# Performance work log

Measured on AMD Instinct MI355X. Metric: run time of the kernel, lower is better.

The kernel has to match this reference:

```python
import jax, jax.numpy as jnp
import numpy as np

V, N, D, HEADS = 4, 1536, 256, 4


def setup_inputs() -> dict:
    key = jax.random.key(0)
    ks = jax.random.split(key, 8)
    s = 0.05  # weight init scale
    return {
        "H": jax.random.normal(ks[0], (V, N, D), jnp.float32),
        "C": jax.random.normal(ks[1], (V, V, N, N), jnp.float32),
        "WQ": jax.random.normal(ks[2], (V, D, D), jnp.float32) * s,
        "WK": jax.random.normal(ks[3], (V, D, D), jnp.float32) * s,
        "WV": jax.random.normal(ks[4], (V, D, D), jnp.float32) * s,
        "in_proj_w": jax.random.normal(ks[5], (3 * D, D), jnp.float32) * s,
        "in_proj_b": jnp.zeros((3 * D,), jnp.float32),
        "out_proj_w": jax.random.normal(ks[6], (D, D), jnp.float32) * s,
        "out_proj_b": jnp.zeros((D,), jnp.float32),
        "alphas": jnp.full((V,), 0.95, jnp.float32),
        "alpha_align": jnp.asarray(0.5, jnp.float32),
        "beta": jnp.asarray(0.5, jnp.float32),
        "topk": 32,
    }


def _ircva(H, in_proj_w, in_proj_b, out_proj_w, out_proj_b, alphas):
    # torch MultiheadAttention, seq=V, batch=N, embed=D, heads=HEADS
    dh = D // HEADS
    qkv = jnp.einsum('snd,ed->sne', H, in_proj_w) + in_proj_b  # (V,N,3D)
    q, k, v = jnp.split(qkv, 3, axis=-1)
    q = q.reshape(V, N, HEADS, dh)
    k = k.reshape(V, N, HEADS, dh)
    v = v.reshape(V, N, HEADS, dh)
    att = jnp.einsum('snhd,tnhd->nhst', q, k) / jnp.sqrt(jnp.float32(dh))
    w = jax.nn.softmax(att, axis=-1)
    o = jnp.einsum('nhst,tnhd->snhd', w, v).reshape(V, N, D)
    fusion = jnp.einsum('snd,ed->sne', o, out_proj_w) + out_proj_b
    a = alphas[:, None, None]
    return fusion * a + (1.0 - a) * H  # (V,N,D)


def _crcva(aligned, C, WQ, WK, WV, K):
    # per-view projections: Linear y = x @ W.T
    Qn = jnp.einsum('vnd,ved->vne', aligned, WQ)
    Kn = jnp.einsum('vnd,ved->vne', aligned, WK)
    Vn = jnp.einsum('vnd,ved->vne', aligned, WV)
    # per-row top-k sparsification of C[p,q]
    vals, idx = jax.lax.top_k(C, K)  # (V,V,N,K)
    Cf = C.reshape(-1, N)
    rows = jnp.arange(Cf.shape[0])[:, None]
    sparse = jnp.zeros_like(Cf).at[rows, idx.reshape(-1, K)].set(vals.reshape(-1, K))
    sparse = sparse.reshape(V, V, N, N)
    row_sum = sparse.sum(axis=-1, keepdims=True) + 1e-12
    C_hat = sparse / row_sum
    # diagonal (p==q) pairs are left as zeros in the torch code
    offdiag = (1.0 - jnp.eye(V, dtype=C.dtype))[:, :, None, None]
    C_hat = C_hat * offdiag
    mask = (C_hat > 0).astype(C.dtype)
    scores = jnp.einsum('pnd,qmd->pqnm', Qn, Kn) / jnp.sqrt(jnp.float32(D))
    scores = scores * mask + (1.0 - mask) * (-1e9)
    alpha_nbr = jax.nn.softmax(scores, axis=-1)
    return jnp.einsum('pqnm,qmd->pnd', alpha_nbr, Vn)  # (V,N,D)


def reference(H, C, WQ, WK, WV, in_proj_w, in_proj_b, out_proj_w, out_proj_b,
              alphas, alpha_align, beta, topk):
    aligned = _ircva(H, in_proj_w, in_proj_b, out_proj_w, out_proj_b, alphas)
    nbr = _crcva(aligned, C, WQ, WK, WV, int(topk))
    a = jax.nn.sigmoid(alpha_align)
    f_fuse = jax.nn.relu(a * aligned + (1.0 - a) * nbr)
    return beta * H + (1.0 - beta) * f_fuse  # (V,N,D)
```

## Files before the change

kernel.cpp:

```cpp
#include <hip/hip_runtime.h>
#include <hip/hip_bf16.h>
#include <math.h>

typedef __bf16 bf16x8 __attribute__((ext_vector_type(8)));
typedef __bf16 bf16x4 __attribute__((ext_vector_type(4)));
typedef float  f32x4  __attribute__((ext_vector_type(4)));

static constexpr int kV = 4;
static constexpr int kN = 1536;
static constexpr int kD = 256;
static constexpr int kTopK = 32;

__global__ __launch_bounds__(256) void convert_kernel(
    const float* __restrict__ H, const float* __restrict__ inW,
    const float* __restrict__ outW, const float* __restrict__ WQ,
    const float* __restrict__ WK, const float* __restrict__ WV,
    __bf16* __restrict__ Hb, __bf16* __restrict__ inWb,
    __bf16* __restrict__ outWb, __bf16* __restrict__ Wqkvb)
{
    int idx = (blockIdx.x * 256 + threadIdx.x) * 4;
    const float* src; __bf16* dst; int off;
    if      (idx < 1572864) { src = H;    dst = Hb;             off = idx; }
    else if (idx < 1769472) { src = inW;  dst = inWb;           off = idx - 1572864; }
    else if (idx < 1835008) { src = outW; dst = outWb;          off = idx - 1769472; }
    else if (idx < 2097152) { src = WQ;   dst = Wqkvb;          off = idx - 1835008; }
    else if (idx < 2359296) { src = WK;   dst = Wqkvb + 262144; off = idx - 2097152; }
    else                    { src = WV;   dst = Wqkvb + 524288; off = idx - 2359296; }
    f32x4 v = *(const f32x4*)(src + off);
    bf16x4 b;
#pragma unroll
    for (int j = 0; j < 4; ++j) b[j] = (__bf16)v[j];
    *(bf16x4*)(dst + off) = b;
}

template<int MT>
__global__ __launch_bounds__(256) void gemm16(
    const __bf16* __restrict__ A, const __bf16* __restrict__ Bm,
    const float* __restrict__ bias, int Nc, int K, int mode,
    __bf16* __restrict__ outB, float* __restrict__ outF,
    const float* __restrict__ Hres, const float* __restrict__ alphas,
    int rowsPerView)
{
    int wave = blockIdx.x * 4 + (threadIdx.x >> 6);
    int tilesN4 = Nc >> 6;
    int tm  = wave / tilesN4;
    int tn4 = wave - tm * tilesN4;
    int lane = threadIdx.x & 63;
    int r    = lane & 15;
    int quad = lane >> 4;
    const __bf16* Ap = A + (size_t)(tm * 16 * MT + r) * K + quad * 8;
    const __bf16* Bp = Bm + (size_t)(tn4 * 64 + r) * K + quad * 8;
    f32x4 acc[MT][4] = {};
    for (int k0 = 0; k0 < K; k0 += 32) {
        bf16x8 a[MT];
#pragma unroll
        for (int mt = 0; mt < MT; ++mt)
            a[mt] = *(const bf16x8*)(Ap + (size_t)mt * 16 * K + k0);
#pragma unroll
        for (int t = 0; t < 4; ++t) {
            bf16x8 b = *(const bf16x8*)(Bp + (size_t)t * 16 * K + k0);
#pragma unroll
            for (int mt = 0; mt < MT; ++mt)
                acc[mt][t] = __builtin_amdgcn_mfma_f32_16x16x32_bf16(a[mt], b, acc[mt][t], 0, 0, 0);
        }
    }
#pragma unroll
    for (int t = 0; t < 4; ++t) {
        int gn = tn4 * 64 + t * 16 + r;
        float bv = bias ? bias[gn] : 0.f;
#pragma unroll
        for (int mt = 0; mt < MT; ++mt)
#pragma unroll
            for (int i = 0; i < 4; ++i) {
                int gm = tm * 16 * MT + mt * 16 + quad * 4 + i;
                float v = acc[mt][t][i] + bv;
                size_t off = (size_t)gm * Nc + gn;
                if (mode == 0) {
                    outB[off] = (__bf16)v;
                } else {
                    float a_ = alphas[gm / rowsPerView];
                    float res = a_ * v + (1.f - a_) * Hres[off];
                    outF[off] = res;
                    outB[off] = (__bf16)res;
                }
            }
    }
}

__global__ __launch_bounds__(256) void gemm_qkv3_kernel(
    const __bf16* __restrict__ A, const __bf16* __restrict__ W,
    __bf16* __restrict__ O0, __bf16* __restrict__ O1, __bf16* __restrict__ O2)
{
    __bf16* Ob = (blockIdx.y == 0) ? O0 : (blockIdx.y == 1) ? O1 : O2;
    const __bf16* Wb = W + (size_t)blockIdx.y * 4 * 65536;
    int wave = blockIdx.x * 4 + (threadIdx.x >> 6);
    int tm  = wave >> 2;
    int tn4 = wave & 3;
    int lane = threadIdx.x & 63;
    int r    = lane & 15;
    int quad = lane >> 4;
    const __bf16* Ap = A + (size_t)(tm * 16 + r) * kD + quad * 8;
    const __bf16* Bp = Wb + (size_t)(tm / 96) * 65536 + (size_t)(tn4 * 64 + r) * kD + quad * 8;
    f32x4 acc[4] = {};
    for (int k0 = 0; k0 < kD; k0 += 32) {
        bf16x8 a = *(const bf16x8*)(Ap + k0);
#pragma unroll
        for (int t = 0; t < 4; ++t) {
            bf16x8 b = *(const bf16x8*)(Bp + (size_t)t * 16 * kD + k0);
            acc[t] = __builtin_amdgcn_mfma_f32_16x16x32_bf16(a, b, acc[t], 0, 0, 0);
        }
    }
#pragma unroll
    for (int t = 0; t < 4; ++t) {
        int gn = tn4 * 64 + t * 16 + r;
#pragma unroll
        for (int i = 0; i < 4; ++i) {
            int gm = tm * 16 + quad * 4 + i;
            Ob[(size_t)gm * kD + gn] = (__bf16)acc[t][i];
        }
    }
}

__global__ __launch_bounds__(256) void attn_kernel(const __bf16* __restrict__ qkv,
                                                   __bf16* __restrict__ o)
{
    int n = blockIdx.x;
    int h = threadIdx.x >> 6;
    int d = threadIdx.x & 63;
    float q[4], k[4], vv[4];
#pragma unroll
    for (int s = 0; s < 4; ++s) {
        size_t base = (size_t)(s * kN + n) * 768 + h * 64 + d;
        q[s]  = (float)qkv[base];
        k[s]  = (float)qkv[base + 256];
        vv[s] = (float)qkv[base + 512];
    }
    float att[4][4];
#pragma unroll
    for (int s = 0; s < 4; ++s)
#pragma unroll
        for (int t = 0; t < 4; ++t) {
            float p = q[s] * k[t];
#pragma unroll
            for (int off = 32; off > 0; off >>= 1) p += __shfl_xor(p, off);
            att[s][t] = p * 0.125f;
        }
#pragma unroll
    for (int s = 0; s < 4; ++s) {
        float mx = fmaxf(fmaxf(att[s][0], att[s][1]), fmaxf(att[s][2], att[s][3]));
        float e0 = __expf(att[s][0] - mx), e1 = __expf(att[s][1] - mx);
        float e2 = __expf(att[s][2] - mx), e3 = __expf(att[s][3] - mx);
        float inv = 1.f / (e0 + e1 + e2 + e3);
        float ov = (e0 * vv[0] + e1 * vv[1] + e2 * vv[2] + e3 * vv[3]) * inv;
        o[(size_t)(s * kN + n) * kD + h * 64 + d] = (__bf16)ov;
    }
}

__global__ __launch_bounds__(256) void vmean_kernel(const __bf16* __restrict__ Vn,
                                                    float* __restrict__ Vmean)
{
    int v = blockIdx.x >> 4, chunk = blockIdx.x & 15;
    int d = threadIdx.x;
    float s = 0.f;
    for (int m = chunk * 96; m < chunk * 96 + 96; ++m)
        s += (float)Vn[((size_t)v * kN + m) * kD + d];
    atomicAdd(&Vmean[v * kD + d], s * (1.f / 1536.f));
}

__global__ __launch_bounds__(256) void topk_kernel(const float* __restrict__ C,
                                                   int* __restrict__ idxOut,
                                                   int* __restrict__ cntOut)
{
    int n  = blockIdx.x;
    int pi = blockIdx.y;
    int p  = pi / 3;
    int qi = pi % 3;
    int q  = qi + (qi >= p ? 1 : 0);
    int tid = threadIdx.x, wv = tid >> 6, lane = tid & 63;
    __shared__ unsigned int hist4[4][256];
    __shared__ unsigned int hist[256];
    __shared__ unsigned int s_bin, s_above, s_cnt, s_E;
    __shared__ unsigned int wsum[4];
    const float* row = C + ((size_t)((p * kV + q) * kN + n)) * kN;
    unsigned int key[6];
#pragma unroll
    for (int j = 0; j < 6; ++j) {
        unsigned int u = __float_as_uint(row[tid + j * 256]);
        key[j] = (u & 0x80000000u) ? ~u : (u | 0x80000000u);
    }
#pragma unroll
    for (int b = 0; b < 4; ++b) hist4[b][tid] = 0;
    if (tid == 0) s_cnt = 0;
    __syncthreads();
#pragma unroll
    for (int j = 0; j < 6; ++j) atomicAdd(&hist4[wv][key[j] >> 24], 1u);
    __syncthreads();
    unsigned int pref = 0, need = kTopK;
    if (tid < 64) {
        unsigned int h[4];
#pragma unroll
        for (int k2 = 0; k2 < 4; ++k2)
            h[k2] = hist4[0][lane*4+k2] + hist4[1][lane*4+k2]
                  + hist4[2][lane*4+k2] + hist4[3][lane*4+k2];
        unsigned int s3 = h[3], s2 = h[2] + s3, s1 = h[1] + s2, s0 = h[0] + s1;
        unsigned int run = s0;
#pragma unroll
        for (int off = 1; off < 64; off <<= 1) {
            unsigned int v = __shfl_down(run, off);
            if (lane + off < 64) run += v;
        }
        unsigned int above = run - s0;
        unsigned int suf[4]  = {above+s0, above+s1, above+s2, above+s3};
        unsigned int sufN[4] = {above+s1, above+s2, above+s3, above};
#pragma unroll
        for (int k2 = 0; k2 < 4; ++k2)
            if (suf[k2] >= need && sufN[k2] < need) {
                s_bin = (unsigned int)(lane*4 + k2); s_above = sufN[k2];
            }
    }
    __syncthreads();
    pref |= s_bin << 24;
    need -= s_above;
    __syncthreads();
    for (int pass = 1; pass < 4; ++pass) {
        const int shift = 24 - 8 * pass;
        hist[tid] = 0;
        __syncthreads();
#pragma unroll
        for (int j = 0; j < 6; ++j)
            if (((key[j] ^ pref) >> (shift + 8)) == 0)
                atomicAdd(&hist[(key[j] >> shift) & 255u], 1u);
        __syncthreads();
        if (tid < 64) {
            unsigned int h0 = hist[lane*4+0], h1 = hist[lane*4+1];
            unsigned int h2 = hist[lane*4+2], h3 = hist[lane*4+3];
            unsigned int s3 = h3, s2 = h2 + s3, s1 = h1 + s2, s0 = h0 + s1;
            unsigned int run = s0;
#pragma unroll
            for (int off = 1; off < 64; off <<= 1) {
                unsigned int v = __shfl_down(run, off);
                if (lane + off < 64) run += v;
            }
            unsigned int above = run - s0;
            unsigned int suf[4]  = {above+s0, above+s1, above+s2, above+s3};
            unsigned int sufN[4] = {above+s1, above+s2, above+s3, above};
#pragma unroll
            for (int k2 = 0; k2 < 4; ++k2)
                if (suf[k2] >= need && sufN[k2] < need) {
                    s_bin = (unsigned int)(lane*4 + k2); s_above = sufN[k2];
                }
        }
        __syncthreads();
        pref |= s_bin << shift;
        need -= s_above;
        __syncthreads();
    }
    unsigned int T = pref;
    unsigned int eq = 0;
#pragma unroll
    for (int j = 0; j < 6; ++j) eq += (key[j] == T) ? 1u : 0u;
    hist[tid] = eq;
    __syncthreads();
    if (tid < 64) {
        unsigned int e = hist[tid] + hist[tid+64] + hist[tid+128] + hist[tid+192];
#pragma unroll
        for (int off = 32; off > 0; off >>= 1) e += __shfl_xor(e, off);
        if (tid == 0) s_E = e;
    }
    __syncthreads();
    unsigned int E = s_E;
    int outBase = ((p * kV + q) * kN + n) * kTopK;
    if (E == need) {
#pragma unroll
        for (int j = 0; j < 6; ++j) {
            unsigned int k = key[j];
            if (k >= T && k > 0x80000000u) {
                unsigned int pos = atomicAdd(&s_cnt, 1u);
                idxOut[outBase + pos] = tid + j * 256;
            }
        }
    } else {
        unsigned int before = 0;
        for (int j = 0; j < 6; ++j) {
            bool e = (key[j] == T);
            unsigned long long m = __ballot(e);
            if (lane == 0) wsum[wv] = (unsigned int)__popcll(m);
            __syncthreads();
            unsigned int base = before;
            for (int w2 = 0; w2 < 4; ++w2) if (w2 < wv) base += wsum[w2];
            unsigned int rank = base + (unsigned int)__popcll(m & ((1ull << lane) - 1ull));
            unsigned int k = key[j];
            bool take = (k > T) || (e && rank < need);
            if (take && k > 0x80000000u) {
                unsigned int pos = atomicAdd(&s_cnt, 1u);
                idxOut[outBase + pos] = tid + j * 256;
            }
            before += wsum[0] + wsum[1] + wsum[2] + wsum[3];
            __syncthreads();
        }
    }
    __syncthreads();
    if (tid == 0) cntOut[(p * kV + q) * kN + n] = (int)s_cnt;
}

__global__ __launch_bounds__(256) void fuse_kernel(
    const __bf16* __restrict__ Qn, const __bf16* __restrict__ Kn,
    const __bf16* __restrict__ Vn, const float* __restrict__ Vmean,
    const int* __restrict__ idxBuf, const int* __restrict__ cntBuf,
    const float* __restrict__ alignedF, const float* __restrict__ H,
    const float* __restrict__ alpha_align, const float* __restrict__ beta,
    float* __restrict__ out)
{
    int n = blockIdx.x, p = blockIdx.y, tid = threadIdx.x;
    __shared__ float qsh[kD];
    __shared__ float wsh[96];
    __shared__ int   osh[96];
    __shared__ float part[4][kD];
    qsh[tid] = (float)Qn[((size_t)p * kN + n) * kD + tid];
    __syncthreads();
    if (tid < 192) {
        int j = tid >> 1, half = tid & 1;
        int g = j >> 5, r = j & 31;
        int q = g + (g >= p ? 1 : 0);
        int cnt = cntBuf[(p * kV + q) * kN + n];
        bool valid = (r < cnt);
        int m = valid ? idxBuf[((p * kV + q) * kN + n) * kTopK + r] : 0;
        int off = valid ? (q * kN + m) * kD : 0;
        float s = 0.f;
        if (valid) {
            const __bf16* kr = Kn + off + half * 128;
            const float*  qh = qsh + half * 128;
            float a0 = 0.f, a1 = 0.f, a2 = 0.f, a3 = 0.f;
#pragma unroll
            for (int dd = 0; dd < 128; dd += 32) {
                bf16x8 k0 = *(const bf16x8*)(kr + dd);
                bf16x8 k1 = *(const bf16x8*)(kr + dd + 8);
                bf16x8 k2 = *(const bf16x8*)(kr + dd + 16);
                bf16x8 k3 = *(const bf16x8*)(kr + dd + 24);
                const float* q0 = qh + dd;
#pragma unroll
                for (int e = 0; e < 8; ++e) {
                    a0 += q0[e]      * (float)k0[e];
                    a1 += q0[e + 8]  * (float)k1[e];
                    a2 += q0[e + 16] * (float)k2[e];
                    a3 += q0[e + 24] * (float)k3[e];
                }
            }
            s = (a0 + a1) + (a2 + a3);
        }
        s += __shfl_xor(s, 1);
        float sc = valid ? s * 0.0625f : -1e30f;
        float mx = sc;
#pragma unroll
        for (int o2 = 2; o2 <= 32; o2 <<= 1) mx = fmaxf(mx, __shfl_xor(mx, o2));
        float e = valid ? __expf(sc - mx) : 0.f;
        float ss = e;
#pragma unroll
        for (int o2 = 2; o2 <= 32; o2 <<= 1) ss += __shfl_xor(ss, o2);
        if (half == 0) {
            wsh[j] = (ss > 0.f) ? e / ss : 0.f;
            osh[j] = off;
        }
    }
    __syncthreads();
    {
        int wv = tid >> 6, lane = tid & 63;
        float a0 = 0.f, a1 = 0.f, a2 = 0.f, a3 = 0.f;
#pragma unroll
        for (int jj = 0; jj < 24; ++jj) {
            int j = wv * 24 + jj;
            float w_ = wsh[j];
            bf16x4 v = *(const bf16x4*)(Vn + osh[j] + lane * 4);
            a0 += w_ * (float)v[0]; a1 += w_ * (float)v[1];
            a2 += w_ * (float)v[2]; a3 += w_ * (float)v[3];
        }
        part[wv][lane * 4 + 0] = a0; part[wv][lane * 4 + 1] = a1;
        part[wv][lane * 4 + 2] = a2; part[wv][lane * 4 + 3] = a3;
    }
    __syncthreads();
    float acc = Vmean[p * kD + tid]
              + part[0][tid] + part[1][tid] + part[2][tid] + part[3][tid];
    float aa = 1.f / (1.f + __expf(-alpha_align[0]));
    float bt = beta[0];
    size_t off = ((size_t)p * kN + n) * kD + tid;
    float al = alignedF[off];
    float f  = fmaxf(aa * al + (1.f - aa) * acc, 0.f);
    out[off] = H[off] * bt + (1.f - bt) * f;
}

extern "C" void kernel_launch(void* const* d_in, const int* in_sizes, int n_in,
                              void* d_out, int out_size, void* d_ws, size_t ws_size,
                              hipStream_t stream)
{
    const float* H        = (const float*)d_in[0];
    const float* C        = (const float*)d_in[1];
    const float* WQ       = (const float*)d_in[2];
    const float* WK       = (const float*)d_in[3];
    const float* WV       = (const float*)d_in[4];
    const float* inW      = (const float*)d_in[5];
    const float* inB      = (const float*)d_in[6];
    const float* outW     = (const float*)d_in[7];
    const float* outBias  = (const float*)d_in[8];
    const float* alphas   = (const float*)d_in[9];
    const float* alpha_al = (const float*)d_in[10];
    const float* beta     = (const float*)d_in[11];
    float* out = (float*)d_out;

    char* w = (char*)d_ws;
    __bf16* Hb       = (__bf16*)w;  w += (size_t)6144 * 256 * 2;
    __bf16* inWb     = (__bf16*)w;  w += (size_t)768 * 256 * 2;
    __bf16* outWb    = (__bf16*)w;  w += (size_t)256 * 256 * 2;
    __bf16* Wqkvb    = (__bf16*)w;  w += (size_t)3 * 4 * 256 * 256 * 2;
    __bf16* qkv      = (__bf16*)w;  w += (size_t)6144 * 768 * 2;
    __bf16* ob       = (__bf16*)w;  w += (size_t)6144 * 256 * 2;
    __bf16* alignedB = (__bf16*)w;  w += (size_t)6144 * 256 * 2;
    float*  alignedF = (float*)w;   w += (size_t)6144 * 256 * 4;
    __bf16* Qn       = (__bf16*)w;  w += (size_t)6144 * 256 * 2;
    __bf16* Kn       = (__bf16*)w;  w += (size_t)6144 * 256 * 2;
    __bf16* Vn       = (__bf16*)w;  w += (size_t)6144 * 256 * 2;
    float*  Vmean    = (float*)w;   w += (size_t)4 * 256 * 4;
    int*    idxBuf   = (int*)w;     w += (size_t)16 * 1536 * 32 * 4;
    int*    cntBuf   = (int*)w;

    hipMemsetAsync(Vmean, 0, 4 * 256 * 4, stream);
    convert_kernel<<<2560, 256, 0, stream>>>(H, inW, outW, WQ, WK, WV,
                                             Hb, inWb, outWb, Wqkvb);
    gemm16<2><<<576, 256, 0, stream>>>(Hb, inWb, inB, 768, 256,
        0, qkv, nullptr, nullptr, nullptr, 0);
    attn_kernel<<<1536, 256, 0, stream>>>(qkv, ob);
    gemm16<1><<<384, 256, 0, stream>>>(ob, outWb, outBias, 256, 256,
        1, alignedB, alignedF, H, alphas, 1536);
    gemm_qkv3_kernel<<<dim3(384, 3), 256, 0, stream>>>(alignedB, Wqkvb, Qn, Kn, Vn);
    vmean_kernel<<<64, 256, 0, stream>>>(Vn, Vmean);
    topk_kernel<<<dim3(1536, 12), 256, 0, stream>>>(C, idxBuf, cntBuf);
    fuse_kernel<<<dim3(1536, 4), 256, 0, stream>>>(Qn, Kn, Vn, Vmean, idxBuf, cntBuf,
        alignedF, H, alpha_al, beta, out);
}
```

Measured before the change: 408.6 us.

## Fuse top-k selection into CRCVA kernel and merge attention with out-projection

```diff
diff --git a/kernel.cpp b/kernel.cpp
--- a/kernel.cpp
+++ b/kernel.cpp
@@ -16,8 +16,13 @@
     const float* __restrict__ outW, const float* __restrict__ WQ,
     const float* __restrict__ WK, const float* __restrict__ WV,
     __bf16* __restrict__ Hb, __bf16* __restrict__ inWb,
-    __bf16* __restrict__ outWb, __bf16* __restrict__ Wqkvb)
-{
+    __bf16* __restrict__ outWb, __bf16* __restrict__ Wqkvb,
+    float* __restrict__ Vmean)
+{
+    if (blockIdx.x == 0) {
+        f32x4 z = {0.f, 0.f, 0.f, 0.f};
+        *(f32x4*)(Vmean + threadIdx.x * 4) = z;
+    }
     int idx = (blockIdx.x * 256 + threadIdx.x) * 4;
     const float* src; __bf16* dst; int off;
     if      (idx < 1572864) { src = H;    dst = Hb;             off = idx; }
@@ -33,298 +38,261 @@
     *(bf16x4*)(dst + off) = b;
 }
 
-template<int MT>
-__global__ __launch_bounds__(256) void gemm16(
+__global__ __launch_bounds__(256) void gemm_qkv_kernel(
     const __bf16* __restrict__ A, const __bf16* __restrict__ Bm,
-    const float* __restrict__ bias, int Nc, int K, int mode,
-    __bf16* __restrict__ outB, float* __restrict__ outF,
-    const float* __restrict__ Hres, const float* __restrict__ alphas,
-    int rowsPerView)
-{
+    const float* __restrict__ bias, __bf16* __restrict__ outB)
+{
+    const int Nc = 768, K = 256;
     int wave = blockIdx.x * 4 + (threadIdx.x >> 6);
-    int tilesN4 = Nc >> 6;
-    int tm  = wave / tilesN4;
-    int tn4 = wave - tm * tilesN4;
+    int tm  = wave / 12;
+    int tn4 = wave - tm * 12;
     int lane = threadIdx.x & 63;
     int r    = lane & 15;
     int quad = lane >> 4;
-    const __bf16* Ap = A + (size_t)(tm * 16 * MT + r) * K + quad * 8;
+    const __bf16* Ap = A + (size_t)(tm * 32 + r) * K + quad * 8;
     const __bf16* Bp = Bm + (size_t)(tn4 * 64 + r) * K + quad * 8;
-    f32x4 acc[MT][4] = {};
+    f32x4 acc[2][4] = {};
     for (int k0 = 0; k0 < K; k0 += 32) {
-        bf16x8 a[MT];
-#pragma unroll
-        for (int mt = 0; mt < MT; ++mt)
-            a[mt] = *(const bf16x8*)(Ap + (size_t)mt * 16 * K + k0);
+        bf16x8 a0 = *(const bf16x8*)(Ap + k0);
+        bf16x8 a1 = *(const bf16x8*)(Ap + (size_t)16 * K + k0);
 #pragma unroll
         for (int t = 0; t < 4; ++t) {
             bf16x8 b = *(const bf16x8*)(Bp + (size_t)t * 16 * K + k0);
-#pragma unroll
-            for (int mt = 0; mt < MT; ++mt)
-                acc[mt][t] = __builtin_amdgcn_mfma_f32_16x16x32_bf16(a[mt], b, acc[mt][t], 0, 0, 0);
+            acc[0][t] = __builtin_amdgcn_mfma_f32_16x16x32_bf16(a0, b, acc[0][t], 0, 0, 0);
+            acc[1][t] = __builtin_amdgcn_mfma_f32_16x16x32_bf16(a1, b, acc[1][t], 0, 0, 0);
         }
     }
 #pragma unroll
     for (int t = 0; t < 4; ++t) {
         int gn = tn4 * 64 + t * 16 + r;
-        float bv = bias ? bias[gn] : 0.f;
-#pragma unroll
-        for (int mt = 0; mt < MT; ++mt)
+        float bv = bias[gn];
+#pragma unroll
+        for (int mt = 0; mt < 2; ++mt)
 #pragma unroll
             for (int i = 0; i < 4; ++i) {
-                int gm = tm * 16 * MT + mt * 16 + quad * 4 + i;
-                float v = acc[mt][t][i] + bv;
-                size_t off = (size_t)gm * Nc + gn;
-                if (mode == 0) {
-                    outB[off] = (__bf16)v;
-                } else {
-                    float a_ = alphas[gm / rowsPerView];
-                    float res = a_ * v + (1.f - a_) * Hres[off];
-                    outF[off] = res;
-                    outB[off] = (__bf16)res;
-                }
-            }
+                int gm = tm * 32 + mt * 16 + quad * 4 + i;
+                outB[(size_t)gm * Nc + gn] = (__bf16)(acc[mt][t][i] + bv);
+            }
+    }
+}
+
+__global__ __launch_bounds__(256) void attg3_kernel(
+    const __bf16* __restrict__ qkv, const __bf16* __restrict__ outWb,
+    const float* __restrict__ outBias, const float* __restrict__ H,
+    const float* __restrict__ alphas,
+    float* __restrict__ alignedF, __bf16* __restrict__ alignedB)
+{
+    __shared__ __bf16 obuf[16][280];
+    int n0 = blockIdx.x * 4;
+    int tid = threadIdx.x;
+    int h = tid >> 6, d = tid & 63;
+#pragma unroll
+    for (int ni = 0; ni < 4; ++ni) {
+        int n = n0 + ni;
+        float q[4], k[4], vv[4];
+#pragma unroll
+        for (int s = 0; s < 4; ++s) {
+            size_t base = (size_t)(s * kN + n) * 768 + h * 64 + d;
+            q[s]  = (float)qkv[base];
+            k[s]  = (float)qkv[base + 256];
+            vv[s] = (float)qkv[base + 512];
+        }
+        float att[4][4];
+#pragma unroll
+        for (int s = 0; s < 4; ++s)
+#pragma unroll
+            for (int t = 0; t < 4; ++t) {
+                float p = q[s] * k[t];
+#pragma unroll
+                for (int off = 32; off > 0; off >>= 1) p += __shfl_xor(p, off);
+                att[s][t] = p * 0.125f;
+            }
+#pragma unroll
+        for (int s = 0; s < 4; ++s) {
+            float mx = fmaxf(fmaxf(att[s][0], att[s][1]), fmaxf(att[s][2], att[s][3]));
+            float e0 = __expf(att[s][0] - mx), e1 = __expf(att[s][1] - mx);
+            float e2 = __expf(att[s][2] - mx), e3 = __expf(att[s][3] - mx);
+            float inv = 1.f / (e0 + e1 + e2 + e3);
+            float ov = (e0 * vv[0] + e1 * vv[1] + e2 * vv[2] + e3 * vv[3]) * inv;
+            obuf[s * 4 + ni][h * 64 + d] = (__bf16)ov;
+        }
+    }
+    __syncthreads();
+    int w = tid >> 6, lane = tid & 63;
+    int r = lane & 15, quad = lane >> 4;
+    f32x4 acc[4] = {};
+    for (int k0 = 0; k0 < 256; k0 += 32) {
+        bf16x8 a = *(const bf16x8*)&obuf[r][quad * 8 + k0];
+#pragma unroll
+        for (int t = 0; t < 4; ++t) {
+            bf16x8 b = *(const bf16x8*)(outWb + (size_t)(w * 64 + t * 16 + r) * 256 + quad * 8 + k0);
+            acc[t] = __builtin_amdgcn_mfma_f32_16x16x32_bf16(a, b, acc[t], 0, 0, 0);
+        }
+    }
+#pragma unroll
+    for (int t = 0; t < 4; ++t) {
+        int gn = w * 64 + t * 16 + r;
+        float bv = outBias[gn];
+#pragma unroll
+        for (int i = 0; i < 4; ++i) {
+            int rl = quad * 4 + i;
+            int s = rl >> 2, ni = rl & 3;
+            size_t gr = (size_t)(s * kN + n0 + ni);
+            float a_ = alphas[s];
+            size_t off = gr * kD + gn;
+            float res = a_ * (acc[t][i] + bv) + (1.f - a_) * H[off];
+            alignedF[off] = res;
+            alignedB[off] = (__bf16)res;
+        }
     }
 }
 
 __global__ __launch_bounds__(256) void gemm_qkv3_kernel(
     const __bf16* __restrict__ A, const __bf16* __restrict__ W,
-    __bf16* __restrict__ O0, __bf16* __restrict__ O1, __bf16* __restrict__ O2)
-{
-    __bf16* Ob = (blockIdx.y == 0) ? O0 : (blockIdx.y == 1) ? O1 : O2;
-    const __bf16* Wb = W + (size_t)blockIdx.y * 4 * 65536;
-    int wave = blockIdx.x * 4 + (threadIdx.x >> 6);
-    int tm  = wave >> 2;
-    int tn4 = wave & 3;
+    __bf16* __restrict__ O0, __bf16* __restrict__ O1, __bf16* __restrict__ O2,
+    float* __restrict__ Vmean)
+{
+    int proj = blockIdx.y;
+    __bf16* Ob = (proj == 0) ? O0 : (proj == 1) ? O1 : O2;
+    const __bf16* Wb = W + (size_t)proj * 4 * 65536;
+    int b = blockIdx.x;
+    int view = b / 48;
+    int tn4 = threadIdx.x >> 6;
     int lane = threadIdx.x & 63;
-    int r    = lane & 15;
-    int quad = lane >> 4;
-    const __bf16* Ap = A + (size_t)(tm * 16 + r) * kD + quad * 8;
-    const __bf16* Bp = Wb + (size_t)(tm / 96) * 65536 + (size_t)(tn4 * 64 + r) * kD + quad * 8;
-    f32x4 acc[4] = {};
+    int r = lane & 15, quad = lane >> 4;
+    const __bf16* Ap = A + (size_t)(b * 32 + r) * kD + quad * 8;
+    const __bf16* Bp = Wb + (size_t)view * 65536 + (size_t)(tn4 * 64 + r) * kD + quad * 8;
+    f32x4 acc[2][4] = {};
     for (int k0 = 0; k0 < kD; k0 += 32) {
-        bf16x8 a = *(const bf16x8*)(Ap + k0);
+        bf16x8 a0 = *(const bf16x8*)(Ap + k0);
+        bf16x8 a1 = *(const bf16x8*)(Ap + (size_t)16 * kD + k0);
 #pragma unroll
         for (int t = 0; t < 4; ++t) {
-            bf16x8 b = *(const bf16x8*)(Bp + (size_t)t * 16 * kD + k0);
-            acc[t] = __builtin_amdgcn_mfma_f32_16x16x32_bf16(a, b, acc[t], 0, 0, 0);
+            bf16x8 bb = *(const bf16x8*)(Bp + (size_t)t * 16 * kD + k0);
+            acc[0][t] = __builtin_amdgcn_mfma_f32_16x16x32_bf16(a0, bb, acc[0][t], 0, 0, 0);
+            acc[1][t] = __builtin_amdgcn_mfma_f32_16x16x32_bf16(a1, bb, acc[1][t], 0, 0, 0);
         }
     }
 #pragma unroll
     for (int t = 0; t < 4; ++t) {
         int gn = tn4 * 64 + t * 16 + r;
 #pragma unroll
-        for (int i = 0; i < 4; ++i) {
-            int gm = tm * 16 + quad * 4 + i;
-            Ob[(size_t)gm * kD + gn] = (__bf16)acc[t][i];
-        }
-    }
-}
-
-__global__ __launch_bounds__(256) void attn_kernel(const __bf16* __restrict__ qkv,
-                                                   __bf16* __restrict__ o)
-{
-    int n = blockIdx.x;
-    int h = threadIdx.x >> 6;
-    int d = threadIdx.x & 63;
-    float q[4], k[4], vv[4];
-#pragma unroll
-    for (int s = 0; s < 4; ++s) {
-        size_t base = (size_t)(s * kN + n) * 768 + h * 64 + d;
-        q[s]  = (float)qkv[base];
-        k[s]  = (float)qkv[base + 256];
-        vv[s] = (float)qkv[base + 512];
-    }
-    float att[4][4];
-#pragma unroll
-    for (int s = 0; s < 4; ++s)
+        for (int mt = 0; mt < 2; ++mt)
+#pragma unroll
+            for (int i = 0; i < 4; ++i) {
+                int gm = b * 32 + mt * 16 + quad * 4 + i;
+                Ob[(size_t)gm * kD + gn] = (__bf16)acc[mt][t][i];
+            }
+    }
+    if (proj == 2) {
 #pragma unroll
         for (int t = 0; t < 4; ++t) {
-            float p = q[s] * k[t];
-#pragma unroll
-            for (int off = 32; off > 0; off >>= 1) p += __shfl_xor(p, off);
-            att[s][t] = p * 0.125f;
-        }
-#pragma unroll
-    for (int s = 0; s < 4; ++s) {
-        float mx = fmaxf(fmaxf(att[s][0], att[s][1]), fmaxf(att[s][2], att[s][3]));
-        float e0 = __expf(att[s][0] - mx), e1 = __expf(att[s][1] - mx);
-        float e2 = __expf(att[s][2] - mx), e3 = __expf(att[s][3] - mx);
-        float inv = 1.f / (e0 + e1 + e2 + e3);
-        float ov = (e0 * vv[0] + e1 * vv[1] + e2 * vv[2] + e3 * vv[3]) * inv;
-        o[(size_t)(s * kN + n) * kD + h * 64 + d] = (__bf16)ov;
-    }
-}
-
-__global__ __launch_bounds__(256) void vmean_kernel(const __bf16* __restrict__ Vn,
-                                                    float* __restrict__ Vmean)
-{
-    int v = blockIdx.x >> 4, chunk = blockIdx.x & 15;
-    int d = threadIdx.x;
-    float s = 0.f;
-    for (int m = chunk * 96; m < chunk * 96 + 96; ++m)
-        s += (float)Vn[((size_t)v * kN + m) * kD + d];
-    atomicAdd(&Vmean[v * kD + d], s * (1.f / 1536.f));
-}
-
-__global__ __launch_bounds__(256) void topk_kernel(const float* __restrict__ C,
-                                                   int* __restrict__ idxOut,
-                                                   int* __restrict__ cntOut)
-{
-    int n  = blockIdx.x;
-    int pi = blockIdx.y;
-    int p  = pi / 3;
-    int qi = pi % 3;
-    int q  = qi + (qi >= p ? 1 : 0);
-    int tid = threadIdx.x, wv = tid >> 6, lane = tid & 63;
-    __shared__ unsigned int hist4[4][256];
-    __shared__ unsigned int hist[256];
-    __shared__ unsigned int s_bin, s_above, s_cnt, s_E;
-    __shared__ unsigned int wsum[4];
-    const float* row = C + ((size_t)((p * kV + q) * kN + n)) * kN;
-    unsigned int key[6];
-#pragma unroll
-    for (int j = 0; j < 6; ++j) {
-        unsigned int u = __float_as_uint(row[tid + j * 256]);
-        key[j] = (u & 0x80000000u) ? ~u : (u | 0x80000000u);
-    }
-#pragma unroll
-    for (int b = 0; b < 4; ++b) hist4[b][tid] = 0;
-    if (tid == 0) s_cnt = 0;
-    __syncthreads();
-#pragma unroll
-    for (int j = 0; j < 6; ++j) atomicAdd(&hist4[wv][key[j] >> 24], 1u);
-    __syncthreads();
-    unsigned int pref = 0, need = kTopK;
-    if (tid < 64) {
-        unsigned int h[4];
-#pragma unroll
-        for (int k2 = 0; k2 < 4; ++k2)
-            h[k2] = hist4[0][lane*4+k2] + hist4[1][lane*4+k2]
-                  + hist4[2][lane*4+k2] + hist4[3][lane*4+k2];
-        unsigned int s3 = h[3], s2 = h[2] + s3, s1 = h[1] + s2, s0 = h[0] + s1;
-        unsigned int run = s0;
-#pragma unroll
-        for (int off = 1; off < 64; off <<= 1) {
-            unsigned int v = __shfl_down(run, off);
-            if (lane + off < 64) run += v;
-        }
-        unsigned int above = run - s0;
-        unsigned int suf[4]  = {above+s0, above+s1, above+s2, above+s3};
-        unsigned int sufN[4] = {above+s1, above+s2, above+s3, above};
-#pragma unroll
-        for (int k2 = 0; k2 < 4; ++k2)
-            if (suf[k2] >= need && sufN[k2] < need) {
-                s_bin = (unsigned int)(lane*4 + k2); s_above = sufN[k2];
-            }
-    }
-    __syncthreads();
-    pref |= s_bin << 24;
-    need -= s_above;
-    __syncthreads();
-    for (int pass = 1; pass < 4; ++pass) {
-        const int shift = 24 - 8 * pass;
-        hist[tid] = 0;
-        __syncthreads();
-#pragma unroll
-        for (int j = 0; j < 6; ++j)
-            if (((key[j] ^ pref) >> (shift + 8)) == 0)
-                atomicAdd(&hist[(key[j] >> shift) & 255u], 1u);
-        __syncthreads();
-        if (tid < 64) {
-            unsigned int h0 = hist[lane*4+0], h1 = hist[lane*4+1];
-            unsigned int h2 = hist[lane*4+2], h3 = hist[lane*4+3];
-            unsigned int s3 = h3, s2 = h2 + s3, s1 = h1 + s2, s0 = h0 + s1;
-            unsigned int run = s0;
-#pragma unroll
-            for (int off = 1; off < 64; off <<= 1) {
-                unsigned int v = __shfl_down(run, off);
-                if (lane + off < 64) run += v;
-            }
-            unsigned int above = run - s0;
-            unsigned int suf[4]  = {above+s0, above+s1, above+s2, above+s3};
-            unsigned int sufN[4] = {above+s1, above+s2, above+s3, above};
-#pragma unroll
-            for (int k2 = 0; k2 < 4; ++k2)
-                if (suf[k2] >= need && sufN[k2] < need) {
-                    s_bin = (unsigned int)(lane*4 + k2); s_above = sufN[k2];
-                }
-        }
-        __syncthreads();
-        pref |= s_bin << shift;
-        need -= s_above;
-        __syncthreads();
-    }
-    unsigned int T = pref;
-    unsigned int eq = 0;
-#pragma unroll
-    for (int j = 0; j < 6; ++j) eq += (key[j] == T) ? 1u : 0u;
-    hist[tid] = eq;
-    __syncthreads();
-    if (tid < 64) {
-        unsigned int e = hist[tid] + hist[tid+64] + hist[tid+128] + hist[tid+192];
-#pragma unroll
-        for (int off = 32; off > 0; off >>= 1) e += __shfl_xor(e, off);
-        if (tid == 0) s_E = e;
-    }
-    __syncthreads();
-    unsigned int E = s_E;
-    int outBase = ((p * kV + q) * kN + n) * kTopK;
-    if (E == need) {
-#pragma unroll
-        for (int j = 0; j < 6; ++j) {
-            unsigned int k = key[j];
-            if (k >= T && k > 0x80000000u) {
-                unsigned int pos = atomicAdd(&s_cnt, 1u);
-                idxOut[outBase + pos] = tid + j * 256;
-            }
-        }
-    } else {
-        unsigned int before = 0;
-        for (int j = 0; j < 6; ++j) {
-            bool e = (key[j] == T);
-            unsigned long long m = __ballot(e);
-            if (lane == 0) wsum[wv] = (unsigned int)__popcll(m);
-            __syncthreads();
-            unsigned int base = before;
-            for (int w2 = 0; w2 < 4; ++w2) if (w2 < wv) base += wsum[w2];
-            unsigned int rank = base + (unsigned int)__popcll(m & ((1ull << lane) - 1ull));
-            unsigned int k = key[j];
-            bool take = (k > T) || (e && rank < need);
-            if (take && k > 0x80000000u) {
-                unsigned int pos = atomicAdd(&s_cnt, 1u);
-                idxOut[outBase + pos] = tid + j * 256;
-            }
-            before += wsum[0] + wsum[1] + wsum[2] + wsum[3];
-            __syncthreads();
-        }
-    }
-    __syncthreads();
-    if (tid == 0) cntOut[(p * kV + q) * kN + n] = (int)s_cnt;
-}
-
-__global__ __launch_bounds__(256) void fuse_kernel(
+            float cs = 0.f;
+#pragma unroll
+            for (int mt = 0; mt < 2; ++mt)
+#pragma unroll
+                for (int i = 0; i < 4; ++i) cs += acc[mt][t][i];
+            cs += __shfl_xor(cs, 16);
+            cs += __shfl_xor(cs, 32);
+            if (quad == 0)
+                atomicAdd(&Vmean[view * kD + tn4 * 64 + t * 16 + r], cs * (1.f / 1536.f));
+        }
+    }
+}
+
+__global__ __launch_bounds__(256) void crcva_kernel(
+    const float* __restrict__ C,
     const __bf16* __restrict__ Qn, const __bf16* __restrict__ Kn,
     const __bf16* __restrict__ Vn, const float* __restrict__ Vmean,
-    const int* __restrict__ idxBuf, const int* __restrict__ cntBuf,
     const float* __restrict__ alignedF, const float* __restrict__ H,
     const float* __restrict__ alpha_align, const float* __restrict__ beta,
     float* __restrict__ out)
 {
     int n = blockIdx.x, p = blockIdx.y, tid = threadIdx.x;
+    int w = tid >> 6, lane = tid & 63;
+    __shared__ unsigned int hist[3][256];
+    __shared__ unsigned int idxl[3][kTopK];
+    __shared__ unsigned int scnt[3];
     __shared__ float qsh[kD];
     __shared__ float wsh[96];
     __shared__ int   osh[96];
     __shared__ float part[4][kD];
-    qsh[tid] = (float)Qn[((size_t)p * kN + n) * kD + tid];
+
+    if (w < 3) {
+        int q = w + (w >= p ? 1 : 0);
+        const float* row = C + ((size_t)((p * kV + q) * kN + n)) * kN;
+        unsigned int key[24];
+#pragma unroll
+        for (int j = 0; j < 24; ++j) {
+            unsigned int u = __float_as_uint(row[j * 64 + lane]);
+            key[j] = (u & 0x80000000u) ? ~u : (u | 0x80000000u);
+        }
+        if (lane == 0) scnt[w] = 0;
+        unsigned int pref = 0, need = kTopK;
+#pragma unroll
+        for (int pass = 0; pass < 4; ++pass) {
+            const int shift = 24 - 8 * pass;
+#pragma unroll
+            for (int k2 = 0; k2 < 4; ++k2) hist[w][lane + k2 * 64] = 0;
+            __builtin_amdgcn_wave_barrier();
+#pragma unroll
+            for (int j = 0; j < 24; ++j) {
+                unsigned int k = key[j];
+                bool match = (pass == 0) || (((k ^ pref) >> (shift + 8)) == 0);
+                if (match) atomicAdd(&hist[w][(k >> shift) & 255u], 1u);
+            }
+            __builtin_amdgcn_wave_barrier();
+            unsigned int h0 = hist[w][lane*4+0], h1 = hist[w][lane*4+1];
+            unsigned int h2 = hist[w][lane*4+2], h3 = hist[w][lane*4+3];
+            unsigned int s3 = h3, s2 = h2 + s3, s1 = h1 + s2, s0 = h0 + s1;
+            unsigned int run = s0;
+#pragma unroll
+            for (int off = 1; off < 64; off <<= 1) {
+                unsigned int v = __shfl_down(run, off);
+                if (lane + off < 64) run += v;
+            }
+            unsigned int above = run - s0;
+            unsigned int suf[4]  = {above+s0, above+s1, above+s2, above+s3};
+            unsigned int sufN[4] = {above+s1, above+s2, above+s3, above};
+            unsigned int pk = 0;
+#pragma unroll
+            for (int k2 = 0; k2 < 4; ++k2)
+                if (suf[k2] >= need && sufN[k2] < need)
+                    pk = ((unsigned int)(lane*4 + k2) << 16) | sufN[k2];
+#pragma unroll
+            for (int off = 1; off < 64; off <<= 1) pk |= __shfl_xor(pk, off);
+            pref |= (pk >> 16) << shift;
+            need -= (pk & 0xffffu);
+        }
+        unsigned int T = pref;
+        unsigned int eqBefore = 0;
+#pragma unroll
+        for (int j = 0; j < 24; ++j) {
+            unsigned int k = key[j];
+            bool e = (k == T);
+            unsigned long long m = __ballot(e);
+            unsigned int rank = eqBefore + (unsigned int)__popcll(m & ((1ull << lane) - 1ull));
+            bool take = (k > T) || (e && rank < need);
+            if (take && k > 0x80000000u) {
+                unsigned int pos = atomicAdd(&scnt[w], 1u);
+                idxl[w][pos] = (unsigned int)(j * 64 + lane);
+            }
+            eqBefore += (unsigned int)__popcll(m);
+        }
+    } else {
+        bf16x4 qv = *(const bf16x4*)(Qn + ((size_t)p * kN + n) * kD + lane * 4);
+#pragma unroll
+        for (int e = 0; e < 4; ++e) qsh[lane * 4 + e] = (float)qv[e];
+    }
     __syncthreads();
+
     if (tid < 192) {
         int j = tid >> 1, half = tid & 1;
         int g = j >> 5, r = j & 31;
         int q = g + (g >= p ? 1 : 0);
-        int cnt = cntBuf[(p * kV + q) * kN + n];
+        int cnt = (int)scnt[g];
         bool valid = (r < cnt);
-        int m = valid ? idxBuf[((p * kV + q) * kN + n) * kTopK + r] : 0;
+        int m = valid ? (int)idxl[g][r] : 0;
         int off = valid ? (q * kN + m) * kD : 0;
         float s = 0.f;
         if (valid) {
@@ -363,21 +331,27 @@
         }
     }
     __syncthreads();
+
     {
-        int wv = tid >> 6, lane = tid & 63;
-        float a0 = 0.f, a1 = 0.f, a2 = 0.f, a3 = 0.f;
-#pragma unroll
-        for (int jj = 0; jj < 24; ++jj) {
-            int j = wv * 24 + jj;
-            float w_ = wsh[j];
-            bf16x4 v = *(const bf16x4*)(Vn + osh[j] + lane * 4);
-            a0 += w_ * (float)v[0]; a1 += w_ * (float)v[1];
-            a2 += w_ * (float)v[2]; a3 += w_ * (float)v[3];
-        }
-        part[wv][lane * 4 + 0] = a0; part[wv][lane * 4 + 1] = a1;
-        part[wv][lane * 4 + 2] = a2; part[wv][lane * 4 + 3] = a3;
+        int half32 = lane >> 5, l32 = lane & 31;
+        float a[8] = {};
+#pragma unroll
+        for (int it = 0; it < 12; ++it) {
+            int j = w * 24 + it * 2 + half32;
+            float wt = wsh[j];
+            bf16x8 v = *(const bf16x8*)(Vn + osh[j] + l32 * 8);
+#pragma unroll
+            for (int e = 0; e < 8; ++e) a[e] += wt * (float)v[e];
+        }
+#pragma unroll
+        for (int e = 0; e < 8; ++e) a[e] += __shfl_xor(a[e], 32);
+        if (half32 == 0) {
+#pragma unroll
+            for (int e = 0; e < 8; ++e) part[w][l32 * 8 + e] = a[e];
+        }
     }
     __syncthreads();
+
     float acc = Vmean[p * kD + tid]
               + part[0][tid] + part[1][tid] + part[2][tid] + part[3][tid];
     float aa = 1.f / (1.f + __expf(-alpha_align[0]));
@@ -412,27 +386,20 @@
     __bf16* outWb    = (__bf16*)w;  w += (size_t)256 * 256 * 2;
     __bf16* Wqkvb    = (__bf16*)w;  w += (size_t)3 * 4 * 256 * 256 * 2;
     __bf16* qkv      = (__bf16*)w;  w += (size_t)6144 * 768 * 2;
-    __bf16* ob       = (__bf16*)w;  w += (size_t)6144 * 256 * 2;
     __bf16* alignedB = (__bf16*)w;  w += (size_t)6144 * 256 * 2;
     float*  alignedF = (float*)w;   w += (size_t)6144 * 256 * 4;
     __bf16* Qn       = (__bf16*)w;  w += (size_t)6144 * 256 * 2;
     __bf16* Kn       = (__bf16*)w;  w += (size_t)6144 * 256 * 2;
     __bf16* Vn       = (__bf16*)w;  w += (size_t)6144 * 256 * 2;
     float*  Vmean    = (float*)w;   w += (size_t)4 * 256 * 4;
-    int*    idxBuf   = (int*)w;     w += (size_t)16 * 1536 * 32 * 4;
-    int*    cntBuf   = (int*)w;
-
-    hipMemsetAsync(Vmean, 0, 4 * 256 * 4, stream);
+
     convert_kernel<<<2560, 256, 0, stream>>>(H, inW, outW, WQ, WK, WV,
-                                             Hb, inWb, outWb, Wqkvb);
-    gemm16<2><<<576, 256, 0, stream>>>(Hb, inWb, inB, 768, 256,
-        0, qkv, nullptr, nullptr, nullptr, 0);
-    attn_kernel<<<1536, 256, 0, stream>>>(qkv, ob);
-    gemm16<1><<<384, 256, 0, stream>>>(ob, outWb, outBias, 256, 256,
-        1, alignedB, alignedF, H, alphas, 1536);
-    gemm_qkv3_kernel<<<dim3(384, 3), 256, 0, stream>>>(alignedB, Wqkvb, Qn, Kn, Vn);
-    vmean_kernel<<<64, 256, 0, stream>>>(Vn, Vmean);
-    topk_kernel<<<dim3(1536, 12), 256, 0, stream>>>(C, idxBuf, cntBuf);
-    fuse_kernel<<<dim3(1536, 4), 256, 0, stream>>>(Qn, Kn, Vn, Vmean, idxBuf, cntBuf,
+                                             Hb, inWb, outWb, Wqkvb, Vmean);
+    gemm_qkv_kernel<<<576, 256, 0, stream>>>(Hb, inWb, inB, qkv);
+    attg3_kernel<<<384, 256, 0, stream>>>(qkv, outWb, outBias, H, alphas,
+                                          alignedF, alignedB);
+    gemm_qkv3_kernel<<<dim3(192, 3), 256, 0, stream>>>(alignedB, Wqkvb,
+                                                       Qn, Kn, Vn, Vmean);
+    crcva_kernel<<<dim3(1536, 4), 256, 0, stream>>>(C, Qn, Kn, Vn, Vmean,
         alignedF, H, alpha_al, beta, out);
 }
```

Result: faster. 377.7 us (-7.6%).
